# Kernel optimization log

Measured on AMD Instinct MI355X. Metric: run time of the kernel, lower is better.

The kernel has to match this reference:

```python
import math
import jax, jax.numpy as jnp
import numpy as np

L, B, N, D, H, DFF = 4, 64, 511, 256, 8, 512
S = N + 1          # +1 game token
HD = D // H
BW = 7             # BOARD_WIDTH (undefined global in source; board-game policy width)


def layer_norm(x, g, b):
    m = jnp.mean(x, axis=-1, keepdims=True)
    v = jnp.var(x, axis=-1, keepdims=True)
    return (x - m) / jnp.sqrt(v + 1e-5) * g + b


def setup_inputs() -> dict:
    key = jax.random.key(0)
    ks = jax.random.split(key, 24)

    def p(k, shape):
        return jax.random.normal(k, shape, jnp.float32) * 0.02

    return {
        "cell_states": jax.random.randint(ks[0], (B * N,), 0, 3, dtype=jnp.int32),
        "edge_type_matrix": jax.random.randint(ks[1], (B, N, N), 0, 3, dtype=jnp.int32),
        "patch_emb": p(ks[2], (3, D)),
        "game_token": p(ks[3], (1, 1, D)),
        "edge_emb": p(ks[4], (3, H)),   # zeros in source init; random here to exercise bias path
        "in_w": p(ks[5], (L, 3 * D, D)), "in_b": p(ks[6], (L, 3 * D)),
        "out_w": p(ks[7], (L, D, D)), "out_b": p(ks[8], (L, D)),
        "ff1_w": p(ks[9], (L, DFF, D)), "ff1_b": p(ks[10], (L, DFF)),
        "ff2_w": p(ks[11], (L, D, DFF)), "ff2_b": p(ks[12], (L, D)),
        "ln1_g": jnp.ones((L, D)), "ln1_b": jnp.zeros((L, D)),
        "ln2_g": jnp.ones((L, D)), "ln2_b": jnp.zeros((L, D)),
        "fc1_w": p(ks[13], (64, D)), "fc1_b": p(ks[14], (64,)),
        "pol_w": p(ks[15], (BW, 64)), "pol_b": p(ks[16], (BW,)),
        "val_w": p(ks[17], (1, 64)), "val_b": p(ks[18], (1,)),
    }


def reference(cell_states, edge_type_matrix, patch_emb, game_token, edge_emb,
              in_w, in_b, out_w, out_b, ff1_w, ff1_b, ff2_w, ff2_b,
              ln1_g, ln1_b, ln2_g, ln2_b, fc1_w, fc1_b, pol_w, pol_b, val_w, val_b):
    # embed cells and prepend game token -> [B, S, D]
    x = patch_emb[cell_states].reshape(B, N, D)
    x = jnp.concatenate([jnp.broadcast_to(game_token, (B, 1, D)), x], axis=1)

    # edge bias: [B,N,N,H] -> [B,H,N,N], pad token row/col with zeros -> [B,H,S,S]
    bias = jnp.transpose(edge_emb[edge_type_matrix], (0, 3, 1, 2))
    bias = jnp.pad(bias, ((0, 0), (0, 0), (1, 0), (1, 0)))

    scale = math.sqrt(HD)
    for i in range(L):
        h = layer_norm(x, ln1_g[i], ln1_b[i])
        qkv = h @ in_w[i].T + in_b[i]                       # [B,S,3D]
        q, k, v = jnp.split(qkv, 3, axis=-1)
        q = q.reshape(B, S, H, HD).transpose(0, 2, 1, 3)    # [B,H,S,HD]
        k = k.reshape(B, S, H, HD).transpose(0, 2, 1, 3)
        v = v.reshape(B, S, H, HD).transpose(0, 2, 1, 3)
        scores = jnp.einsum('bhqd,bhkd->bhqk', q, k) / scale + bias
        attn = jax.nn.softmax(scores, axis=-1)              # dropout = identity (eval)
        o = jnp.einsum('bhqk,bhkd->bhqd', attn, v)
        o = o.transpose(0, 2, 1, 3).reshape(B, S, D)
        x = x + (o @ out_w[i].T + out_b[i])
        h2 = layer_norm(x, ln2_g[i], ln2_b[i])
        x = x + (jax.nn.relu(h2 @ ff1_w[i].T + ff1_b[i]) @ ff2_w[i].T + ff2_b[i])

    g = x[:, 0, :]
    o = jax.nn.relu(g @ fc1_w.T + fc1_b)
    policy_logits = o @ pol_w.T + pol_b
    value = jnp.tanh(o @ val_w.T + val_b)
    return policy_logits, value
```

## Files before the change

### kernel.cpp

```cpp
#include <hip/hip_runtime.h>
#include <hip/hip_bf16.h>
#include <math.h>

#define L_ 4
#define B_ 64
#define N_ 511
#define D_ 256
#define H_ 8
#define DFF_ 512
#define S_ 512
#define HD_ 32
#define BW_ 7
#define BS_ (B_*S_)

typedef __attribute__((ext_vector_type(8))) short short8;
typedef __attribute__((ext_vector_type(4))) short short4v;
typedef __attribute__((ext_vector_type(4))) float f32x4;

#define L2E 1.44269504088896340f
#define QSCL (0.17677669529663687f * 1.44269504088896340f)

#if defined(__HIP_DEVICE_COMPILE__) && __has_builtin(__builtin_amdgcn_exp2f)
#define EXP2(x) __builtin_amdgcn_exp2f(x)
#else
#define EXP2(x) exp2f(x)
#endif

__device__ inline ushort f2b(float f) {
    unsigned u = __float_as_uint(f);
    unsigned r = (u + 0x7fffu + ((u >> 16) & 1u)) >> 16;
    return (ushort)r;
}

__device__ inline float b2f(ushort u) {
    return __uint_as_float(((uint)u) << 16);
}

#if defined(__HIP_DEVICE_COMPILE__) && __has_builtin(__builtin_amdgcn_cvt_pk_bf16_f32)
typedef __attribute__((ext_vector_type(2))) __bf16 bf16x2_t;
__device__ inline uint pk_bf16(float a, float b) {
    bf16x2_t r = __builtin_amdgcn_cvt_pk_bf16_f32(a, b);
    return *(uint*)&r;
}
#else
__device__ inline uint pk_bf16(float a, float b) {
    return (uint)f2b(a) | ((uint)f2b(b) << 16);
}
#endif

__device__ inline f32x4 bsel4v(uint E, uint tlo, uint thi) {
    f32x4 r;
#if defined(__HIP_DEVICE_COMPILE__) && __has_builtin(__builtin_amdgcn_perm)
    uint E2  = E + E;
    uint E2b = E2 | 0x01010101u;
    uint s01 = __builtin_amdgcn_perm(E2b, E2, 0x05010400u);
    uint s23 = __builtin_amdgcn_perm(E2b, E2, 0x07030602u);
    uint p01 = __builtin_amdgcn_perm(thi, tlo, s01);
    uint p23 = __builtin_amdgcn_perm(thi, tlo, s23);
    r[0] = __uint_as_float(p01 << 16);
    r[1] = __uint_as_float(p01 & 0xFFFF0000u);
    r[2] = __uint_as_float(p23 << 16);
    r[3] = __uint_as_float(p23 & 0xFFFF0000u);
#else
    #pragma unroll
    for (int i = 0; i < 4; i++) {
        unsigned char e = (unsigned char)((E >> (8 * i)) & 0xff);
        uint bb = e == 0 ? (tlo & 0xFFFFu) : (e == 1 ? (tlo >> 16) :
                  (e == 2 ? (thi & 0xFFFFu) : 0u));
        r[i] = __uint_as_float(bb << 16);
    }
#endif
    return r;
}

__device__ inline void gload16(const void* g, void* l) {
#if __has_builtin(__builtin_amdgcn_global_load_lds)
    __builtin_amdgcn_global_load_lds(
        (const __attribute__((address_space(1))) void*)g,
        (__attribute__((address_space(3))) void*)l, 16, 0, 0);
#else
    *(short8*)l = *(const short8*)g;
#endif
}

__global__ __launch_bounds__(256) void build_ln(const int* __restrict__ cs,
                                                const float* __restrict__ patch,
                                                const float* __restrict__ game,
                                                const float* __restrict__ gw,
                                                const float* __restrict__ bw,
                                                float* __restrict__ x,
                                                ushort* __restrict__ h)
{
    int t = threadIdx.x;
    int lane = t & 63;
    int wv = t >> 6;
    int row = blockIdx.x * 4 + wv;
    int s = row & (S_ - 1);
    float4 v;
    if (s == 0) {
        v = ((const float4*)game)[lane];
    } else {
        int b = row >> 9;
        int cell = cs[b * N_ + s - 1];
        v = ((const float4*)(patch + cell * D_))[lane];
    }
    ((float4*)x)[(size_t)row * 64 + lane] = v;

    float sm = v.x + v.y + v.z + v.w;
    #pragma unroll
    for (int o = 32; o >= 1; o >>= 1) sm += __shfl_xor(sm, o);
    float mean = sm * (1.f / 256.f);
    float dx = v.x - mean, dy = v.y - mean, dz = v.z - mean, dw = v.w - mean;
    float s2 = dx * dx + dy * dy + dz * dz + dw * dw;
    #pragma unroll
    for (int o = 32; o >= 1; o >>= 1) s2 += __shfl_xor(s2, o);
    float rstd = rsqrtf(s2 * (1.f / 256.f) + 1e-5f);
    float4 g  = *(const float4*)(gw + lane * 4);
    float4 bb = *(const float4*)(bw + lane * 4);
    ushort4 o4;
    o4.x = f2b(dx * rstd * g.x + bb.x);
    o4.y = f2b(dy * rstd * g.y + bb.y);
    o4.z = f2b(dz * rstd * g.z + bb.z);
    o4.w = f2b(dw * rstd * g.w + bb.w);
    *(ushort4*)(h + (size_t)row * D_ + lane * 4) = o4;
}

__global__ __launch_bounds__(256) void build_et8(const int* __restrict__ et,
                                                 unsigned char* __restrict__ et8)
{
    long idx = (long)blockIdx.x * 256 + threadIdx.x;
    int k = (int)(idx & (S_ - 1));
    long rem = idx >> 9;
    int q = (int)(rem & (S_ - 1));
    int b = (int)(rem >> 9);
    unsigned char v = 3;
    if (q > 0 && k > 0) {
        v = (unsigned char)et[((long)b * N_ + (q - 1)) * N_ + (k - 1)];
    }
    et8[idx] = v;
}

__global__ __launch_bounds__(256) void convert_all(const float* __restrict__ in_w,
                                                   const float* __restrict__ out_w,
                                                   const float* __restrict__ ff1_w,
                                                   const float* __restrict__ ff2_w,
                                                   ushort* __restrict__ inwb,
                                                   ushort* __restrict__ outwb,
                                                   ushort* __restrict__ ff1wb,
                                                   ushort* __restrict__ ff2wb)
{
    int i = blockIdx.x * 256 + threadIdx.x;
    const float* src;
    ushort* dst;
    int j;
    float s = 1.f;
    if (i < 196608) {
        j = i; src = in_w; dst = inwb;
        int r = (j >> 6) % 768;
        if (r < 256) s = (float)QSCL;
    } else if (i < 262144) {
        j = i - 196608; src = out_w; dst = outwb;
    } else if (i < 393216) {
        j = i - 262144; src = ff1_w; dst = ff1wb;
    } else {
        j = i - 393216; src = ff2_w; dst = ff2wb;
    }
    float4 v = ((const float4*)src)[j];
    ushort4 o4;
    o4.x = f2b(v.x * s); o4.y = f2b(v.y * s); o4.z = f2b(v.z * s); o4.w = f2b(v.w * s);
    ((ushort4*)dst)[j] = o4;
}

template<int K, int NT, bool RELU, bool QSC, bool QKV>
__global__ __launch_bounds__(256, 2) void gemm_lds(const ushort* __restrict__ A,
                                                   const ushort* __restrict__ W,
                                                   const float* __restrict__ bias,
                                                   ushort* __restrict__ Cout,
                                                   ushort* __restrict__ Kb,
                                                   ushort* __restrict__ Vt)
{
    __shared__ ushort As[2][4096];
    __shared__ ushort Ws[2][4096];
    const int N = NT * 128;
    int t = threadIdx.x;
    int wave = t >> 6, lane = t & 63;
    int lr = lane & 15, quad = lane >> 4;
    int lk = quad * 8;
    int blk = blockIdx.x;
    int xcd = blk & 7, idx = blk >> 3;
    int m0 = (xcd * 32 + (idx & 31)) * 128;
    int n0 = (idx >> 5) * 128;
    int mh = (wave >> 1) * 64, nh = (wave & 1) * 64;

    const ushort* ga0 = A + (size_t)(m0 + (t >> 2)) * K + (t & 3) * 8;
    const ushort* ga1 = ga0 + (size_t)64 * K;
    const ushort* gw0 = W + (size_t)(n0 + (t >> 2)) * K + (t & 3) * 8;
    const ushort* gw1 = gw0 + (size_t)64 * K;
    int t8 = t * 8;

    f32x4 acc[4][4];
    f32x4 zz = {0.f, 0.f, 0.f, 0.f};
    #pragma unroll
    for (int i = 0; i < 4; i++)
        #pragma unroll
        for (int j = 0; j < 4; j++) acc[i][j] = zz;

    for (int k0 = 0; k0 < K; k0 += 64) {
        gload16(ga0 + k0,      &As[0][t8]);
        gload16(ga1 + k0,      &As[0][t8 + 2048]);
        gload16(ga0 + k0 + 32, &As[1][t8]);
        gload16(ga1 + k0 + 32, &As[1][t8 + 2048]);
        gload16(gw0 + k0,      &Ws[0][t8]);
        gload16(gw1 + k0,      &Ws[0][t8 + 2048]);
        gload16(gw0 + k0 + 32, &Ws[1][t8]);
        gload16(gw1 + k0 + 32, &Ws[1][t8 + 2048]);
        __syncthreads();
        short8 af[2][4], wf[2][4];
        #pragma unroll
        for (int kk = 0; kk < 2; kk++) {
            #pragma unroll
            for (int i = 0; i < 4; i++) af[kk][i] = *(const short8*)&As[kk][(mh + i * 16 + lr) * 32 + lk];
            #pragma unroll
            for (int j = 0; j < 4; j++) wf[kk][j] = *(const short8*)&Ws[kk][(nh + j * 16 + lr) * 32 + lk];
        }
        #pragma unroll
        for (int kk = 0; kk < 2; kk++)
            #pragma unroll
            for (int i = 0; i < 4; i++)
                #pragma unroll
                for (int j = 0; j < 4; j++)
                    acc[i][j] = __builtin_amdgcn_mfma_f32_16x16x32_bf16(af[kk][i], wf[kk][j], acc[i][j], 0, 0, 0);
        __syncthreads();
    }

    #pragma unroll
    for (int nt = 0; nt < 4; nt++) {
        int colbase = n0 + nh + nt * 16;
        int col = colbase + lr;
        float bv = bias[col];
        if (QSC && colbase < 256) bv *= (float)QSCL;
        int region = QKV ? (colbase >> 8) : 0;
        #pragma unroll
        for (int mt = 0; mt < 4; mt++) {
            int rowb = m0 + mh + mt * 16 + quad * 4;
            if (!QKV || region == 0) {
                #pragma unroll
                for (int r = 0; r < 4; r++) {
                    size_t cidx = (size_t)(rowb + r) * N + col;
                    float v = acc[mt][nt][r] + bv;
                    if (RELU) v = fmaxf(v, 0.f);
                    Cout[cidx] = f2b(v);
                }
            } else if (region == 1) {
                int hh = (col >> 5) & 7, d = col & 31;
                int bb = rowb >> 9, s = rowb & 511;
                size_t kbase = ((size_t)(bb * 8 + hh) * 512 + s) * 32 + d;
                #pragma unroll
                for (int r = 0; r < 4; r++)
                    Kb[kbase + (size_t)r * 32] = f2b(acc[mt][nt][r] + bv);
            } else {
                int hh = (col >> 5) & 7, d = col & 31;
                int bb = rowb >> 9, s = rowb & 511;
                ushort4 w;
                w.x = f2b(acc[mt][nt][0] + bv);
                w.y = f2b(acc[mt][nt][1] + bv);
                w.z = f2b(acc[mt][nt][2] + bv);
                w.w = f2b(acc[mt][nt][3] + bv);
                size_t vidx = (((size_t)(bb * 8 + hh) * 32 + (s >> 4)) * 32 + d) * 16 + (s & 15);
                *(ushort4*)&Vt[vidx] = w;
            }
        }
    }
}

template<int K>
__global__ __launch_bounds__(256, 2) void gemm_ln(const ushort* __restrict__ A,
                                                  const ushort* __restrict__ W,
                                                  const float* __restrict__ bias,
                                                  float* __restrict__ X,
                                                  const float* __restrict__ lng,
                                                  const float* __restrict__ lnb,
                                                  ushort* __restrict__ Hout)
{
    __shared__ ushort As[2][2048];
    __shared__ ushort Ws[2][8192];
    __shared__ float lds_s[64][4];
    __shared__ float lds_q[64][4];
    int t = threadIdx.x;
    int wave = t >> 6, lane = t & 63;
    int lr = lane & 15, quad = lane >> 4;
    int lk = quad * 8;
    int blk = blockIdx.x;
    int xcd = blk & 7;
    int m0 = (xcd * 64 + (blk >> 3)) * 64;
    int nh = wave * 64;

    const ushort* ga = A + (size_t)(m0 + (t >> 2)) * K + (t & 3) * 8;
    const ushort* gw = W + (size_t)(t >> 2) * K + (t & 3) * 8;
    int t8 = t * 8;

    f32x4 acc[4][4];
    f32x4 zz = {0.f, 0.f, 0.f, 0.f};
    #pragma unroll
    for (int i = 0; i < 4; i++)
        #pragma unroll
        for (int j = 0; j < 4; j++) acc[i][j] = zz;

    for (int k0 = 0; k0 < K; k0 += 64) {
        gload16(ga + k0,      &As[0][t8]);
        gload16(ga + k0 + 32, &As[1][t8]);
        #pragma unroll
        for (int j = 0; j < 4; j++) {
            gload16(gw + (size_t)(j * 64) * K + k0,      &Ws[0][t8 + j * 2048]);
            gload16(gw + (size_t)(j * 64) * K + k0 + 32, &Ws[1][t8 + j * 2048]);
        }
        __syncthreads();
        short8 af[2][4], wf[2][4];
        #pragma unroll
        for (int kk = 0; kk < 2; kk++) {
            #pragma unroll
            for (int i = 0; i < 4; i++) af[kk][i] = *(const short8*)&As[kk][(i * 16 + lr) * 32 + lk];
            #pragma unroll
            for (int j = 0; j < 4; j++) wf[kk][j] = *(const short8*)&Ws[kk][(nh + j * 16 + lr) * 32 + lk];
        }
        #pragma unroll
        for (int kk = 0; kk < 2; kk++)
            #pragma unroll
            for (int i = 0; i < 4; i++)
                #pragma unroll
                for (int j = 0; j < 4; j++)
                    acc[i][j] = __builtin_amdgcn_mfma_f32_16x16x32_bf16(af[kk][i], wf[kk][j], acc[i][j], 0, 0, 0);
        __syncthreads();
    }

    float gc[4], bc[4], bi[4];
    #pragma unroll
    for (int nt = 0; nt < 4; nt++) {
        int col = nh + nt * 16 + lr;
        gc[nt] = lng[col]; bc[nt] = lnb[col]; bi[nt] = bias[col];
    }
    float psum[16], psq[16];
    #pragma unroll
    for (int e = 0; e < 16; e++) { psum[e] = 0.f; psq[e] = 0.f; }
    #pragma unroll
    for (int nt = 0; nt < 4; nt++) {
        #pragma unroll
        for (int mt = 0; mt < 4; mt++) {
            #pragma unroll
            for (int r = 0; r < 4; r++) {
                int row = m0 + mt * 16 + quad * 4 + r;
                size_t idx = (size_t)row * D_ + nh + nt * 16 + lr;
                float v = acc[mt][nt][r] + bi[nt] + X[idx];
                X[idx] = v;
                acc[mt][nt][r] = v;
                psum[mt * 4 + r] += v;
                psq[mt * 4 + r]  += v * v;
            }
        }
    }
    #pragma unroll
    for (int e = 0; e < 16; e++) {
        float s = psum[e], q = psq[e];
        s += __shfl_xor(s, 1); q += __shfl_xor(q, 1);
        s += __shfl_xor(s, 2); q += __shfl_xor(q, 2);
        s += __shfl_xor(s, 4); q += __shfl_xor(q, 4);
        s += __shfl_xor(s, 8); q += __shfl_xor(q, 8);
        psum[e] = s; psq[e] = q;
    }
    if (lr == 0) {
        #pragma unroll
        for (int mt = 0; mt < 4; mt++)
            #pragma unroll
            for (int r = 0; r < 4; r++) {
                int rl = mt * 16 + quad * 4 + r;
                lds_s[rl][wave] = psum[mt * 4 + r];
                lds_q[rl][wave] = psq[mt * 4 + r];
            }
    }
    __syncthreads();
    #pragma unroll
    for (int mt = 0; mt < 4; mt++) {
        #pragma unroll
        for (int r = 0; r < 4; r++) {
            int rl = mt * 16 + quad * 4 + r;
            f32x4 ss = *(const f32x4*)lds_s[rl];
            f32x4 qq = *(const f32x4*)lds_q[rl];
            float s = ss[0] + ss[1] + ss[2] + ss[3];
            float q = qq[0] + qq[1] + qq[2] + qq[3];
            float mean = s * (1.f / 256.f);
            float rstd = rsqrtf(q * (1.f / 256.f) - mean * mean + 1e-5f);
            int row = m0 + mt * 16 + quad * 4 + r;
            #pragma unroll
            for (int nt = 0; nt < 4; nt++) {
                size_t idx = (size_t)row * D_ + nh + nt * 16 + lr;
                float hv = (acc[mt][nt][r] - mean) * rstd * gc[nt] + bc[nt];
                Hout[idx] = f2b(hv);
            }
        }
    }
}

__global__ __launch_bounds__(256, 4) void attn_mfma(const ushort* __restrict__ qkv,
                                                    const ushort* __restrict__ Kb,
                                                    const ushort* __restrict__ Vt,
                                                    const unsigned char* __restrict__ et8,
                                                    const float* __restrict__ eemb,
                                                    ushort* __restrict__ o)
{
    int t = threadIdx.x;
    int wave = t >> 6, lane = t & 63;
    int lr = lane & 15, quad = lane >> 4;
    int lk = quad * 8;
    int blk = blockIdx.x;
    int b = ((blk >> 8) << 3) | (blk & 7);
    int h = (blk >> 3) & 7;
    int qq = (blk >> 6) & 3;
    int bh = b * 8 + h;
    int q0 = qq * 128 + wave * 32;
    float eb0 = eemb[h] * L2E, eb1 = eemb[8 + h] * L2E, eb2 = eemb[16 + h] * L2E;
    uint tlo = (uint)f2b(eb0) | ((uint)f2b(eb1) << 16);
    uint thi = (uint)f2b(eb2);

    short8 qf[2];
    #pragma unroll
    for (int X = 0; X < 2; X++)
        qf[X] = *(const short8*)(qkv + ((size_t)(b * S_ + q0 + X * 16 + lr)) * 768 + h * 32 + lk);
    int gl = ((lr >> 2) << 3) | (lr & 3);
    const ushort* Kp = Kb + ((size_t)(bh * S_) + gl) * 32 + lk;
    const ushort* Vp = Vt + (size_t)bh * 16384 + (quad >> 1) * 512 + lr * 16 + (quad & 1) * 8;
    const unsigned char* Ep0 = et8 + ((size_t)(b * S_ + q0 + lr)) * 512 + quad * 8;
    const unsigned char* Ep1 = Ep0 + (size_t)16 * 512;

    const short8 vones8 = { (short)0x3F80, (short)0x3F80, (short)0x3F80, (short)0x3F80,
                            (short)0x3F80, (short)0x3F80, (short)0x3F80, (short)0x3F80 };

    f32x4 zz = {0.f, 0.f, 0.f, 0.f};
    f32x4 oacc[2][2], lacc[2];
    #pragma unroll
    for (int X = 0; X < 2; X++) { oacc[X][0] = zz; oacc[X][1] = zz; lacc[X] = zz; }

    short8 kf0 = *(const short8*)(Kp);
    short8 kf1 = *(const short8*)(Kp + 128);
    uint2 e0 = *(const uint2*)(Ep0);
    uint2 e1 = *(const uint2*)(Ep1);
    short8 vb0 = *(const short8*)(Vp);
    short8 vb1 = *(const short8*)(Vp + 256);
    Kp += 1024; Ep0 += 32; Ep1 += 32; Vp += 1024;

    #pragma unroll 2
    for (int it = 0; it < 16; ++it) {
        short8 nk0 = *(const short8*)(Kp);
        short8 nk1 = *(const short8*)(Kp + 128);
        uint2 ne0 = *(const uint2*)(Ep0);
        uint2 ne1 = *(const uint2*)(Ep1);
        short8 nv0 = *(const short8*)(Vp);
        short8 nv1 = *(const short8*)(Vp + 256);
        Kp += 1024; Ep0 += 32; Ep1 += 32; Vp += 1024;
        #pragma unroll
        for (int X = 0; X < 2; X++) {
            uint Ea = X ? e1.x : e0.x;
            uint Eb = X ? e1.y : e0.y;
            f32x4 c0 = bsel4v(Ea, tlo, thi);
            f32x4 c1 = bsel4v(Eb, tlo, thi);
            f32x4 s0 = __builtin_amdgcn_mfma_f32_16x16x32_bf16(kf0, qf[X], c0, 0, 0, 0);
            f32x4 s1 = __builtin_amdgcn_mfma_f32_16x16x32_bf16(kf1, qf[X], c1, 0, 0, 0);
            float p0[4], p1[4];
            #pragma unroll
            for (int r = 0; r < 4; r++) {
                p0[r] = EXP2(s0[r]);
                p1[r] = EXP2(s1[r]);
            }
            union { short8 v; uint u[4]; } PA;
            PA.u[0] = pk_bf16(p0[0], p0[1]); PA.u[1] = pk_bf16(p0[2], p0[3]);
            PA.u[2] = pk_bf16(p1[0], p1[1]); PA.u[3] = pk_bf16(p1[2], p1[3]);
            oacc[X][0] = __builtin_amdgcn_mfma_f32_16x16x32_bf16(PA.v, vb0, oacc[X][0], 0, 0, 0);
            oacc[X][1] = __builtin_amdgcn_mfma_f32_16x16x32_bf16(PA.v, vb1, oacc[X][1], 0, 0, 0);
            lacc[X]    = __builtin_amdgcn_mfma_f32_16x16x32_bf16(PA.v, vones8, lacc[X], 0, 0, 0);
        }
        kf0 = nk0; kf1 = nk1; e0 = ne0; e1 = ne1; vb0 = nv0; vb1 = nv1;
    }

    #pragma unroll
    for (int X = 0; X < 2; X++) {
        #pragma unroll
        for (int r = 0; r < 4; r++) {
            int q = quad * 4 + r;
            float inv = 1.f / lacc[X][r];
            size_t base = (size_t)(b * S_ + q0 + X * 16 + q) * D_ + h * 32;
            o[base + lr]      = f2b(oacc[X][0][r] * inv);
            o[base + 16 + lr] = f2b(oacc[X][1][r] * inv);
        }
    }
}

__global__ __launch_bounds__(64) void attn_last(const ushort* __restrict__ qkv,
                                                const ushort* __restrict__ Kb,
                                                const ushort* __restrict__ Vt,
                                                ushort* __restrict__ o)
{
    int lane = threadIdx.x;
    int bh = blockIdx.x;
    int b = bh >> 3, h = bh & 7;
    __shared__ float ps[512];

    const ushort* qp = qkv + (size_t)(b * S_) * 768 + h * 32;
    float q[32];
    #pragma unroll
    for (int d8 = 0; d8 < 4; d8++) {
        short8 v = *(const short8*)(qp + d8 * 8);
        #pragma unroll
        for (int j = 0; j < 8; j++) q[d8 * 8 + j] = b2f((ushort)v[j]);
    }
    const ushort* kp = Kb + ((size_t)bh * 512 + lane * 8) * 32;
    float lsum = 0.f;
    #pragma unroll
    for (int j = 0; j < 8; j++) {
        float s = 0.f;
        #pragma unroll
        for (int d8 = 0; d8 < 4; d8++) {
            short8 kv = *(const short8*)(kp + j * 32 + d8 * 8);
            #pragma unroll
            for (int e = 0; e < 8; e++) s += q[d8 * 8 + e] * b2f((ushort)kv[e]);
        }
        float pe = b2f(f2b(EXP2(s)));
        ps[lane * 8 + j] = pe;
        lsum += pe;
    }
    #pragma unroll
    for (int off = 32; off >= 1; off >>= 1) lsum += __shfl_xor(lsum, off);
    __syncthreads();

    int d = lane & 31, kh = lane >> 5;
    const ushort* vp = Vt + (size_t)bh * 16384 + d * 16;
    float acc = 0.f;
    for (int k = kh * 256; k < kh * 256 + 256; k += 16) {
        const ushort* vt = vp + (size_t)(k >> 4) * 512;
        #pragma unroll
        for (int e = 0; e < 16; e++) acc += ps[k + e] * b2f(vt[e]);
    }
    acc += __shfl_xor(acc, 32);
    if (lane < 32)
        o[(size_t)(b * S_) * D_ + h * 32 + d] = f2b(acc / lsum);
}

__global__ __launch_bounds__(256) void last_tail(const ushort* __restrict__ ob,
                                                 const ushort* __restrict__ outw,
                                                 const float* __restrict__ outb,
                                                 const float* __restrict__ ln2g,
                                                 const float* __restrict__ ln2b,
                                                 const ushort* __restrict__ ff1w,
                                                 const float* __restrict__ ff1b,
                                                 const ushort* __restrict__ ff2w,
                                                 const float* __restrict__ ff2b,
                                                 float* __restrict__ X)
{
    __shared__ float obs[256];
    __shared__ ushort h2s[256];
    __shared__ ushort ffs[512];
    __shared__ float red[8];
    int t = threadIdx.x;
    int b = blockIdx.x;
    size_t row = (size_t)b * S_;

    obs[t] = b2f(ob[row * D_ + t]);
    __syncthreads();

    const ushort* w0 = outw + (size_t)t * 256;
    float acc = 0.f;
    for (int k8 = 0; k8 < 256; k8 += 8) {
        short8 wv = *(const short8*)(w0 + k8);
        #pragma unroll
        for (int e = 0; e < 8; e++) acc += obs[k8 + e] * b2f((ushort)wv[e]);
    }
    float xv = acc + outb[t] + X[row * D_ + t];

    float s1 = xv, s2 = xv * xv;
    #pragma unroll
    for (int off = 32; off >= 1; off >>= 1) { s1 += __shfl_xor(s1, off); s2 += __shfl_xor(s2, off); }
    int wv_ = t >> 6, lane = t & 63;
    if (lane == 0) { red[wv_] = s1; red[4 + wv_] = s2; }
    __syncthreads();
    float S1 = red[0] + red[1] + red[2] + red[3];
    float S2 = red[4] + red[5] + red[6] + red[7];
    float mean = S1 * (1.f / 256.f);
    float rstd = rsqrtf(S2 * (1.f / 256.f) - mean * mean + 1e-5f);
    h2s[t] = f2b((xv - mean) * rstd * ln2g[t] + ln2b[t]);
    __syncthreads();

    #pragma unroll
    for (int cc = 0; cc < 2; cc++) {
        int col = t + cc * 256;
        const ushort* w1 = ff1w + (size_t)col * 256;
        float a = 0.f;
        for (int k8 = 0; k8 < 256; k8 += 8) {
            short8 wv1 = *(const short8*)(w1 + k8);
            #pragma unroll
            for (int e = 0; e < 8; e++) a += b2f(h2s[k8 + e]) * b2f((ushort)wv1[e]);
        }
        ffs[col] = f2b(fmaxf(a + ff1b[col], 0.f));
    }
    __syncthreads();

    const ushort* w2 = ff2w + (size_t)t * 512;
    float a2 = 0.f;
    for (int k8 = 0; k8 < 512; k8 += 8) {
        short8 wv2 = *(const short8*)(w2 + k8);
        #pragma unroll
        for (int e = 0; e < 8; e++) a2 += b2f(ffs[k8 + e]) * b2f((ushort)wv2[e]);
    }
    X[row * D_ + t] = a2 + ff2b[t] + xv;
}

__global__ __launch_bounds__(64) void head_kernel(const float* __restrict__ x,
                                                  const float* __restrict__ fc1w,
                                                  const float* __restrict__ fc1b,
                                                  const float* __restrict__ polw,
                                                  const float* __restrict__ polb,
                                                  const float* __restrict__ valw,
                                                  const float* __restrict__ valb,
                                                  float* __restrict__ out)
{
    __shared__ float o1[64];
    int b = blockIdx.x;
    int t = threadIdx.x;
    const float* g = x + (size_t)b * S_ * D_;
    float acc = fc1b[t];
    for (int k = 0; k < D_; k++) acc += g[k] * fc1w[t * D_ + k];
    o1[t] = fmaxf(acc, 0.f);
    __syncthreads();
    if (t < BW_) {
        float a = polb[t];
        for (int k = 0; k < 64; k++) a += o1[k] * polw[t * 64 + k];
        out[b * BW_ + t] = a;
    } else if (t == BW_) {
        float a = valb[0];
        for (int k = 0; k < 64; k++) a += o1[k] * valw[k];
        out[B_ * BW_ + b] = tanhf(a);
    }
}

extern "C" void kernel_launch(void* const* d_in, const int* in_sizes, int n_in,
                              void* d_out, int out_size, void* d_ws, size_t ws_size,
                              hipStream_t stream)
{
    const int*   cs    = (const int*)d_in[0];
    const int*   etm   = (const int*)d_in[1];
    const float* patch = (const float*)d_in[2];
    const float* game  = (const float*)d_in[3];
    const float* eemb  = (const float*)d_in[4];
    const float* in_w  = (const float*)d_in[5];
    const float* in_b  = (const float*)d_in[6];
    const float* out_w = (const float*)d_in[7];
    const float* out_b = (const float*)d_in[8];
    const float* ff1_w = (const float*)d_in[9];
    const float* ff1_b = (const float*)d_in[10];
    const float* ff2_w = (const float*)d_in[11];
    const float* ff2_b = (const float*)d_in[12];
    const float* ln1_g = (const float*)d_in[13];
    const float* ln1_b = (const float*)d_in[14];
    const float* ln2_g = (const float*)d_in[15];
    const float* ln2_b = (const float*)d_in[16];
    const float* fc1_w = (const float*)d_in[17];
    const float* fc1_b = (const float*)d_in[18];
    const float* pol_w = (const float*)d_in[19];
    const float* pol_b = (const float*)d_in[20];
    const float* val_w = (const float*)d_in[21];
    const float* val_b = (const float*)d_in[22];
    float* out = (float*)d_out;

    char* base = (char*)d_ws;
    float*  x     = (float*)(base + 0);
    ushort* h     = (ushort*)(base + 33554432);
    ushort* qkvb  = (ushort*)(base + 50331648);
    ushort* Kb    = (ushort*)(base + 100663296);
    ushort* Vt    = (ushort*)(base + 117440512);
    ushort* ob    = (ushort*)(base + 134217728);
    unsigned char* et8 = (unsigned char*)(base + 150994944);
    ushort* inwb  = (ushort*)(base + 167772160);
    ushort* outwb = (ushort*)(base + 169345024);
    ushort* ff1wb = (ushort*)(base + 169869312);
    ushort* ff2wb = (ushort*)(base + 170917888);

    build_et8<<<65536, 256, 0, stream>>>(etm, et8);
    convert_all<<<2048, 256, 0, stream>>>(in_w, out_w, ff1_w, ff2_w,
                                          inwb, outwb, ff1wb, ff2wb);
    build_ln<<<8192, 256, 0, stream>>>(cs, patch, game, ln1_g, ln1_b, x, h);

    for (int i = 0; i < L_; i++) {
        gemm_lds<256, 6, false, true, true><<<1536, 256, 0, stream>>>(
            h, inwb + (size_t)i * 196608, in_b + i * 768, qkvb, Kb, Vt);
        if (i < L_ - 1) {
            attn_mfma<<<2048, 256, 0, stream>>>(qkvb, Kb, Vt, et8, eemb, ob);
            gemm_ln<256><<<512, 256, 0, stream>>>(
                ob, outwb + (size_t)i * 65536, out_b + i * 256, x,
                ln2_g + i * D_, ln2_b + i * D_, h);
            gemm_lds<256, 4, true, false, false><<<1024, 256, 0, stream>>>(
                h, ff1wb + (size_t)i * 131072, ff1_b + i * 512, qkvb, nullptr, nullptr);
            gemm_ln<512><<<512, 256, 0, stream>>>(
                qkvb, ff2wb + (size_t)i * 131072, ff2_b + i * 256, x,
                ln1_g + (i + 1) * D_, ln1_b + (i + 1) * D_, h);
        } else {
            attn_last<<<512, 64, 0, stream>>>(qkvb, Kb, Vt, ob);
            last_tail<<<64, 256, 0, stream>>>(
                ob, outwb + (size_t)i * 65536, out_b + i * 256,
                ln2_g + i * D_, ln2_b + i * D_,
                ff1wb + (size_t)i * 131072, ff1_b + i * 512,
                ff2wb + (size_t)i * 131072, ff2_b + i * 256, x);
        }
    }
    head_kernel<<<B_, 64, 0, stream>>>(x, fc1_w, fc1_b, pol_w, pol_b, val_w, val_b, out);
}
```

Baseline: 689.7 us.

## Skip full-sequence Q projection in last layer and fuse head into tail

```diff
diff --git a/kernel.cpp b/kernel.cpp
--- a/kernel.cpp
+++ b/kernel.cpp
@@ -171,7 +171,7 @@
     ((ushort4*)dst)[j] = o4;
 }
 
-template<int K, int NT, bool RELU, bool QSC, bool QKV>
+template<int K, int NT, bool RELU, bool QSC, bool QKV, int RBASE = 0>
 __global__ __launch_bounds__(256, 2) void gemm_lds(const ushort* __restrict__ A,
                                                    const ushort* __restrict__ W,
                                                    const float* __restrict__ bias,
@@ -239,7 +239,7 @@
         int col = colbase + lr;
         float bv = bias[col];
         if (QSC && colbase < 256) bv *= (float)QSCL;
-        int region = QKV ? (colbase >> 8) : 0;
+        int region = QKV ? ((colbase >> 8) + RBASE) : 0;
         #pragma unroll
         for (int mt = 0; mt < 4; mt++) {
             int rowb = m0 + mh + mt * 16 + quad * 4;
@@ -493,15 +493,38 @@
     }
 }
 
-__global__ __launch_bounds__(64) void attn_last(const ushort* __restrict__ qkv,
-                                                const ushort* __restrict__ Kb,
-                                                const ushort* __restrict__ Vt,
-                                                ushort* __restrict__ o)
-{
-    int lane = threadIdx.x;
+__global__ __launch_bounds__(256) void qg_last(const ushort* __restrict__ h,
+                                               const ushort* __restrict__ inwQ,
+                                               const float* __restrict__ inb,
+                                               ushort* __restrict__ qkvb)
+{
+    __shared__ float hs[256];
+    int t = threadIdx.x;
+    int b = blockIdx.x;
+    size_t row = (size_t)b * S_;
+    hs[t] = b2f(h[row * D_ + t]);
+    __syncthreads();
+    const ushort* w = inwQ + (size_t)t * 256;
+    float acc = 0.f;
+    for (int k8 = 0; k8 < 256; k8 += 8) {
+        short8 wv = *(const short8*)(w + k8);
+        #pragma unroll
+        for (int e = 0; e < 8; e++) acc += hs[k8 + e] * b2f((ushort)wv[e]);
+    }
+    qkvb[row * 768 + t] = f2b(acc + inb[t] * (float)QSCL);
+}
+
+__global__ __launch_bounds__(256) void attn_last(const ushort* __restrict__ qkv,
+                                                 const ushort* __restrict__ Kb,
+                                                 const ushort* __restrict__ Vt,
+                                                 ushort* __restrict__ o)
+{
+    int t = threadIdx.x;
     int bh = blockIdx.x;
     int b = bh >> 3, h = bh & 7;
     __shared__ float ps[512];
+    __shared__ float pv[8][32];
+    __shared__ float red[4];
 
     const ushort* qp = qkv + (size_t)(b * S_) * 768 + h * 32;
     float q[32];
@@ -511,10 +534,10 @@
         #pragma unroll
         for (int j = 0; j < 8; j++) q[d8 * 8 + j] = b2f((ushort)v[j]);
     }
-    const ushort* kp = Kb + ((size_t)bh * 512 + lane * 8) * 32;
+    const ushort* kp = Kb + ((size_t)bh * 512 + t * 2) * 32;
     float lsum = 0.f;
     #pragma unroll
-    for (int j = 0; j < 8; j++) {
+    for (int j = 0; j < 2; j++) {
         float s = 0.f;
         #pragma unroll
         for (int d8 = 0; d8 < 4; d8++) {
@@ -523,24 +546,32 @@
             for (int e = 0; e < 8; e++) s += q[d8 * 8 + e] * b2f((ushort)kv[e]);
         }
         float pe = b2f(f2b(EXP2(s)));
-        ps[lane * 8 + j] = pe;
+        ps[t * 2 + j] = pe;
         lsum += pe;
     }
     #pragma unroll
     for (int off = 32; off >= 1; off >>= 1) lsum += __shfl_xor(lsum, off);
-    __syncthreads();
-
-    int d = lane & 31, kh = lane >> 5;
+    int wv_ = t >> 6, lane = t & 63;
+    if (lane == 0) red[wv_] = lsum;
+    __syncthreads();
+    float denom = red[0] + red[1] + red[2] + red[3];
+
+    int d = t & 31, kh = t >> 5;
     const ushort* vp = Vt + (size_t)bh * 16384 + d * 16;
     float acc = 0.f;
-    for (int k = kh * 256; k < kh * 256 + 256; k += 16) {
+    for (int k = kh * 64; k < kh * 64 + 64; k += 16) {
         const ushort* vt = vp + (size_t)(k >> 4) * 512;
         #pragma unroll
         for (int e = 0; e < 16; e++) acc += ps[k + e] * b2f(vt[e]);
     }
-    acc += __shfl_xor(acc, 32);
-    if (lane < 32)
-        o[(size_t)(b * S_) * D_ + h * 32 + d] = f2b(acc / lsum);
+    pv[kh][d] = acc;
+    __syncthreads();
+    if (t < 32) {
+        float a = 0.f;
+        #pragma unroll
+        for (int g = 0; g < 8; g++) a += pv[g][t];
+        o[(size_t)(b * S_) * D_ + h * 32 + t] = f2b(a / denom);
+    }
 }
 
 __global__ __launch_bounds__(256) void last_tail(const ushort* __restrict__ ob,
@@ -552,12 +583,20 @@
                                                  const float* __restrict__ ff1b,
                                                  const ushort* __restrict__ ff2w,
                                                  const float* __restrict__ ff2b,
-                                                 float* __restrict__ X)
+                                                 const float* __restrict__ X,
+                                                 const float* __restrict__ fc1w,
+                                                 const float* __restrict__ fc1b,
+                                                 const float* __restrict__ polw,
+                                                 const float* __restrict__ polb,
+                                                 const float* __restrict__ valw,
+                                                 const float* __restrict__ valb,
+                                                 float* __restrict__ out)
 {
     __shared__ float obs[256];
     __shared__ ushort h2s[256];
     __shared__ ushort ffs[512];
     __shared__ float red[8];
+    __shared__ float o1s[64];
     int t = threadIdx.x;
     int b = blockIdx.x;
     size_t row = (size_t)b * S_;
@@ -608,33 +647,25 @@
         #pragma unroll
         for (int e = 0; e < 8; e++) a2 += b2f(ffs[k8 + e]) * b2f((ushort)wv2[e]);
     }
-    X[row * D_ + t] = a2 + ff2b[t] + xv;
-}
-
-__global__ __launch_bounds__(64) void head_kernel(const float* __restrict__ x,
-                                                  const float* __restrict__ fc1w,
-                                                  const float* __restrict__ fc1b,
-                                                  const float* __restrict__ polw,
-                                                  const float* __restrict__ polb,
-                                                  const float* __restrict__ valw,
-                                                  const float* __restrict__ valb,
-                                                  float* __restrict__ out)
-{
-    __shared__ float o1[64];
-    int b = blockIdx.x;
-    int t = threadIdx.x;
-    const float* g = x + (size_t)b * S_ * D_;
-    float acc = fc1b[t];
-    for (int k = 0; k < D_; k++) acc += g[k] * fc1w[t * D_ + k];
-    o1[t] = fmaxf(acc, 0.f);
+    float xf = a2 + ff2b[t] + xv;
+    __syncthreads();
+    obs[t] = xf;
+    __syncthreads();
+
+    if (t < 64) {
+        const float* fw = fc1w + (size_t)t * 256;
+        float a = fc1b[t];
+        for (int k = 0; k < 256; k++) a += obs[k] * fw[k];
+        o1s[t] = fmaxf(a, 0.f);
+    }
     __syncthreads();
     if (t < BW_) {
         float a = polb[t];
-        for (int k = 0; k < 64; k++) a += o1[k] * polw[t * 64 + k];
+        for (int k = 0; k < 64; k++) a += o1s[k] * polw[t * 64 + k];
         out[b * BW_ + t] = a;
     } else if (t == BW_) {
         float a = valb[0];
-        for (int k = 0; k < 64; k++) a += o1[k] * valw[k];
+        for (int k = 0; k < 64; k++) a += o1s[k] * valw[k];
         out[B_ * BW_ + b] = tanhf(a);
     }
 }
@@ -687,9 +718,9 @@
     build_ln<<<8192, 256, 0, stream>>>(cs, patch, game, ln1_g, ln1_b, x, h);
 
     for (int i = 0; i < L_; i++) {
-        gemm_lds<256, 6, false, true, true><<<1536, 256, 0, stream>>>(
-            h, inwb + (size_t)i * 196608, in_b + i * 768, qkvb, Kb, Vt);
         if (i < L_ - 1) {
+            gemm_lds<256, 6, false, true, true><<<1536, 256, 0, stream>>>(
+                h, inwb + (size_t)i * 196608, in_b + i * 768, qkvb, Kb, Vt);
             attn_mfma<<<2048, 256, 0, stream>>>(qkvb, Kb, Vt, et8, eemb, ob);
             gemm_ln<256><<<512, 256, 0, stream>>>(
                 ob, outwb + (size_t)i * 65536, out_b + i * 256, x,
@@ -700,13 +731,18 @@
                 qkvb, ff2wb + (size_t)i * 131072, ff2_b + i * 256, x,
                 ln1_g + (i + 1) * D_, ln1_b + (i + 1) * D_, h);
         } else {
-            attn_last<<<512, 64, 0, stream>>>(qkvb, Kb, Vt, ob);
+            gemm_lds<256, 4, false, false, true, 1><<<1024, 256, 0, stream>>>(
+                h, inwb + (size_t)i * 196608 + 65536, in_b + i * 768 + 256,
+                qkvb, Kb, Vt);
+            qg_last<<<64, 256, 0, stream>>>(h, inwb + (size_t)i * 196608,
+                                            in_b + i * 768, qkvb);
+            attn_last<<<512, 256, 0, stream>>>(qkvb, Kb, Vt, ob);
             last_tail<<<64, 256, 0, stream>>>(
                 ob, outwb + (size_t)i * 65536, out_b + i * 256,
                 ln2_g + i * D_, ln2_b + i * D_,
                 ff1wb + (size_t)i * 131072, ff1_b + i * 512,
-                ff2wb + (size_t)i * 131072, ff2_b + i * 256, x);
-        }
-    }
-    head_kernel<<<B_, 64, 0, stream>>>(x, fc1_w, fc1_b, pol_w, pol_b, val_w, val_b, out);
-}
+                ff2wb + (size_t)i * 131072, ff2_b + i * 256, x,
+                fc1_w, fc1_b, pol_w, pol_b, val_w, val_b, out);
+        }
+    }
+}
```

New measurement: 691.4 us (median of 3 runs). About the same (+0.3%).
